# Performance work log

Measured on AMD Instinct MI355X. Metric: run time of the kernel, lower is better.

The kernel has to match this reference:

```python
import jax, jax.numpy as jnp
import numpy as np

N_NODES = 100000


def _gcn_norm(edge_index, num_nodes):
    # PyG gcn_norm with add_self_loops=True, symmetric normalization.
    src = jnp.concatenate([edge_index[0], jnp.arange(num_nodes)])
    dst = jnp.concatenate([edge_index[1], jnp.arange(num_nodes)])
    ones = jnp.ones(src.shape[0], dtype=jnp.float32)
    deg = jax.ops.segment_sum(ones, dst, num_segments=num_nodes)
    dinv = jnp.where(deg > 0, jax.lax.rsqrt(deg), 0.0)
    norm = dinv[src] * dinv[dst]  # [E + N]
    return src, dst, norm


def _gcn_conv(x, W, b, src, dst, norm, num_nodes):
    h = x @ W                                  # dense transform first (PyG order)
    msg = h[src] * norm[:, None]               # gather + scale, [E+N, D]
    agg = jax.ops.segment_sum(msg, dst, num_segments=num_nodes)
    return agg + b


def setup_inputs() -> dict:
    key = jax.random.key(0)
    ks = jax.random.split(key, 6)
    F_in, D, C, E = 256, 64, 47, 1200000
    x = jax.random.normal(ks[0], (N_NODES, F_in), dtype=jnp.float32)
    edge_index = jax.random.randint(ks[1], (2, E), 0, N_NODES)
    W1 = jax.random.normal(ks[2], (F_in, D), dtype=jnp.float32) * (1.0 / np.sqrt(F_in))
    b1 = jnp.zeros((D,), dtype=jnp.float32)
    W2 = jax.random.normal(ks[3], (D, C), dtype=jnp.float32) * (1.0 / np.sqrt(D))
    b2 = jnp.zeros((C,), dtype=jnp.float32)
    return {"x": x, "edge_index": edge_index, "W1": W1, "b1": b1, "W2": W2, "b2": b2}


def reference(x, edge_index, W1, b1, W2, b2):
    src, dst, norm = _gcn_norm(edge_index, N_NODES)
    h = jax.nn.relu(_gcn_conv(x, W1, b1, src, dst, norm, N_NODES))
    # dropout: eval mode (training=False) -> identity
    out = _gcn_conv(h, W2, b2, src, dst, norm, N_NODES)
    return jax.nn.log_softmax(out, axis=1)
```

## Files before the change

kernel.cpp:

```cpp
#include <hip/hip_runtime.h>
#include <math.h>

#define NN 100000
#define FIN 256
#define D1 64
#define C2 47
#define S2 48
#define NBKT 1563
#define CAP 1024
#define EPB 4096

typedef unsigned short u16;
typedef unsigned int u32;
typedef __attribute__((ext_vector_type(8))) short short8;
typedef __attribute__((ext_vector_type(4))) float floatx4;

__device__ __forceinline__ u16 f2b(float f) {
    union { float f; unsigned u; } v; v.f = f;
    unsigned r = v.u + 0x7FFF + ((v.u >> 16) & 1);
    return (u16)(r >> 16);
}
__device__ __forceinline__ float b2f_lo(u32 p) { union { unsigned u; float f; } v; v.u = p << 16; return v.f; }
__device__ __forceinline__ float b2f_hi(u32 p) { union { unsigned u; float f; } v; v.u = p & 0xFFFF0000u; return v.f; }
__device__ __forceinline__ u32 scale2(u32 pair, float dd) {
    return (u32)f2b(dd * b2f_lo(pair)) | ((u32)f2b(dd * b2f_hi(pair)) << 16);
}

__global__ __launch_bounds__(256) void k_pre(
    const float* __restrict__ W1, const float* __restrict__ W2,
    u16* __restrict__ W1t, u16* __restrict__ W2t, int* __restrict__ bucketCnt)
{
    int i = blockIdx.x * 256 + threadIdx.x;
    if (i < FIN * D1) {
        int c = i >> 8, k = i & 255;
        W1t[i] = f2b(W1[k * D1 + c]);
    } else if (i < FIN * D1 + D1 * S2) {
        int j = i - FIN * D1;
        int c = j >> 6, k = j & 63;
        W2t[j] = (c < C2) ? f2b(W2[k * C2 + c]) : (u16)0;
    } else {
        int z = i - (FIN * D1 + D1 * S2);
        if (z < NBKT) bucketCnt[z] = 0;
    }
}

__global__ __launch_bounds__(256) void k_bin_gemm1(
    const int* __restrict__ src, const int* __restrict__ dst, int E, int nScat,
    int* __restrict__ bucketCnt, u32* __restrict__ ebuf,
    const float* __restrict__ x, const u16* __restrict__ W1t,
    u16* __restrict__ h1u)
{
    __shared__ __align__(16) char smraw[20480];
    const int b = blockIdx.x;
    const int t = threadIdx.x;

    if (b < nScat) {
        int* hist = (int*)smraw;
        int* base = (int*)(smraw + 6256);
        for (int i = t; i < NBKT; i += 256) hist[i] = 0;
        __syncthreads();
        int e0 = b * EPB + t;
        u32 pk[16]; int bk[16], tk[16];
        #pragma unroll
        for (int j = 0; j < 16; ++j) {
            int e = e0 + j * 256;
            bk[j] = -1;
            if (e < E) {
                int d = dst[e];
                bk[j] = d >> 6;
                pk[j] = (u32)src[e] | ((u32)(d & 63) << 17);
                tk[j] = atomicAdd(&hist[bk[j]], 1);
            }
        }
        __syncthreads();
        for (int i = t; i < NBKT; i += 256)
            base[i] = hist[i] ? atomicAdd(&bucketCnt[i], hist[i]) : 0;
        __syncthreads();
        #pragma unroll
        for (int j = 0; j < 16; ++j)
            if (bk[j] >= 0) {
                int pos = base[bk[j]] + tk[j];
                if (pos < CAP) ebuf[(size_t)bk[j] * CAP + pos] = pk[j];
            }
        return;
    }

    short (*As)[2560] = (short(*)[2560])(smraw);
    short (*Bs)[2560] = (short(*)[2560])(smraw + 10240);
    const int bm = (b - nScat) * 64;
    const int w = t >> 6, lane = t & 63;
    const int arow = t >> 2;
    const int ak0 = (t & 3) * 8;

    floatx4 acc[4] = {};
    const int gr = bm + arow;
    const bool rowok = gr < NN;
    const float* xrow = x + (size_t)(rowok ? gr : 0) * FIN + ak0;

    float4 v0 = make_float4(0.f,0.f,0.f,0.f), v1 = v0;
    if (rowok) { v0 = *(const float4*)(xrow); v1 = *(const float4*)(xrow + 4); }
    short8 wv = *(const short8*)(W1t + arow * FIN + ak0);
    {
        short8 av;
        av[0]=(short)f2b(v0.x); av[1]=(short)f2b(v0.y); av[2]=(short)f2b(v0.z); av[3]=(short)f2b(v0.w);
        av[4]=(short)f2b(v1.x); av[5]=(short)f2b(v1.y); av[6]=(short)f2b(v1.z); av[7]=(short)f2b(v1.w);
        *(short8*)(&As[0][arow * 40 + ak0]) = av;
        *(short8*)(&Bs[0][arow * 40 + ak0]) = wv;
    }
    __syncthreads();

    int cb_ = 0;
    for (int kt = 32; kt <= FIN; kt += 32) {
        const bool more = kt < FIN;
        float4 n0, n1; short8 nw;
        if (more) {
            if (rowok) { n0 = *(const float4*)(xrow + kt); n1 = *(const float4*)(xrow + kt + 4); }
            else { n0 = make_float4(0.f,0.f,0.f,0.f); n1 = n0; }
            nw = *(const short8*)(W1t + arow * FIN + kt + ak0);
        }
        short8 af = *(const short8*)(&As[cb_][(w * 16 + (lane & 15)) * 40 + (lane >> 4) * 8]);
        #pragma unroll
        for (int cb = 0; cb < 4; ++cb) {
            short8 bv = *(const short8*)(&Bs[cb_][(cb * 16 + (lane & 15)) * 40 + (lane >> 4) * 8]);
            acc[cb] = __builtin_amdgcn_mfma_f32_16x16x32_bf16(af, bv, acc[cb], 0, 0, 0);
        }
        if (!more) break;
        short8 av;
        av[0]=(short)f2b(n0.x); av[1]=(short)f2b(n0.y); av[2]=(short)f2b(n0.z); av[3]=(short)f2b(n0.w);
        av[4]=(short)f2b(n1.x); av[5]=(short)f2b(n1.y); av[6]=(short)f2b(n1.z); av[7]=(short)f2b(n1.w);
        *(short8*)(&As[cb_ ^ 1][arow * 40 + ak0]) = av;
        *(short8*)(&Bs[cb_ ^ 1][arow * 40 + ak0]) = nw;
        __syncthreads();
        cb_ ^= 1;
    }

    #pragma unroll
    for (int cb = 0; cb < 4; ++cb) {
        #pragma unroll
        for (int r = 0; r < 4; ++r) {
            int grow = bm + w * 16 + (lane >> 4) * 4 + r;
            if (grow < NN)
                h1u[(size_t)grow * D1 + cb * 16 + (lane & 15)] = f2b(acc[cb][r]);
        }
    }
}

__global__ __launch_bounds__(256) void k_sort_scale(
    const int* __restrict__ bucketCnt, const u32* __restrict__ ebuf,
    int* __restrict__ rpg, u32* __restrict__ sortedg,
    const u16* __restrict__ h1u, u16* __restrict__ hs1)
{
    __shared__ int hist[64], cur[64];
    __shared__ float dinvs[64];
    const int b = blockIdx.x, t = threadIdx.x, bm = b * 64;

    if (t < 64) hist[t] = 0;
    __syncthreads();
    int cnt = bucketCnt[b]; if (cnt > CAP) cnt = CAP;
    const u32* eb = ebuf + (size_t)b * CAP;
    u32 p[4];
    #pragma unroll
    for (int j = 0; j < 4; ++j) {
        int e = t + j * 256;
        p[j] = 0xFFFFFFFFu;
        if (e < cnt) { p[j] = eb[e]; atomicAdd(&hist[(p[j] >> 17) & 63], 1); }
    }
    __syncthreads();
    if (t < 64) {
        int h = hist[t];
        int v = h;
        #pragma unroll
        for (int off = 1; off < 64; off <<= 1) {
            int u = __shfl_up(v, off);
            if (t >= off) v += u;
        }
        cur[t] = v - h;
        rpg[(size_t)b * 64 + t] = v - h;
        dinvs[t] = rsqrtf((float)h + 1.0f);
    }
    __syncthreads();
    #pragma unroll
    for (int j = 0; j < 4; ++j)
        if (p[j] != 0xFFFFFFFFu) {
            int pos = atomicAdd(&cur[(p[j] >> 17) & 63], 1);
            sortedg[(size_t)b * CAP + pos] = p[j] & 0x1FFFF;
        }

    const uint4* hb = (const uint4*)(h1u + (size_t)bm * D1);
    uint4* ob = (uint4*)(hs1 + (size_t)bm * D1);
    #pragma unroll
    for (int j = 0; j < 2; ++j) {
        int idx = t + j * 256;
        int row = idx >> 3;
        if (bm + row < NN) {
            uint4 v = hb[idx];
            float dd = dinvs[row];
            ob[idx] = make_uint4(scale2(v.x, dd), scale2(v.y, dd),
                                 scale2(v.z, dd), scale2(v.w, dd));
        }
    }
}

__global__ __launch_bounds__(256) void k_gather_gemm2(
    const int* __restrict__ bucketCnt, const int* __restrict__ rpg,
    const u32* __restrict__ sortedg, const u16* __restrict__ hs1,
    const float* __restrict__ b1, const u16* __restrict__ W2t,
    u16* __restrict__ hs2)
{
    __shared__ u32 sorted[CAP];
    __shared__ int rp[65];
    __shared__ short As[2][64 * 40];
    __shared__ short Bs[2][48 * 40];
    __shared__ float b1s[64];
    const int t = threadIdx.x;
    const int b = blockIdx.x, bm = b * 64;
    const int w = t >> 6, lane = t & 63;
    const int g = t >> 3, l8 = t & 7;

    for (int s = t; s < 384; s += 256) {
        int kt = s / 192, rem = s - kt * 192;
        int r = rem >> 2, j = rem & 3;
        *(short8*)(&Bs[kt][r * 40 + j * 8]) =
            *(const short8*)(W2t + r * D1 + kt * 32 + j * 8);
    }
    int cnt = bucketCnt[b]; if (cnt > CAP) cnt = CAP;
    if (t < 64) { b1s[t] = b1[t]; rp[t] = rpg[(size_t)b * 64 + t]; }
    if (t == 0) rp[64] = cnt;
    for (int i = t; i < cnt; i += 256)
        sorted[i] = sortedg[(size_t)b * CAP + i];
    __syncthreads();

    {
        const int col = 8 * l8;
        const int kth = l8 >> 2;
        const int cs  = col & 31;
        float4 bbl = *(const float4*)(b1s + col);
        float4 bbh = *(const float4*)(b1s + col + 4);
        #pragma unroll 1
        for (int i = 0; i < 2; ++i) {
            int rl = g * 2 + i;
            int node = bm + rl;
            if (node >= NN) break;
            int beg = rp[rl], end = rp[rl + 1];
            float dd = rsqrtf((float)(end - beg) + 1.0f);
            uint4 sp = *((const uint4*)(hs1 + (size_t)node * D1) + l8);
            float a0=b2f_lo(sp.x), a1=b2f_hi(sp.x), a2=b2f_lo(sp.y), a3=b2f_hi(sp.y);
            float a4=b2f_lo(sp.z), a5=b2f_hi(sp.z), a6=b2f_lo(sp.w), a7=b2f_hi(sp.w);
            float c0=0.f,c1=0.f,c2=0.f,c3=0.f,c4=0.f,c5=0.f,c6=0.f,c7=0.f;
            int e = beg;
            for (; e + 4 <= end; e += 4) {
                int s0 = sorted[e+0], s1 = sorted[e+1], s2 = sorted[e+2], s3 = sorted[e+3];
                uint4 p0 = *((const uint4*)(hs1 + (size_t)s0 * D1) + l8);
                uint4 p1 = *((const uint4*)(hs1 + (size_t)s1 * D1) + l8);
                uint4 p2 = *((const uint4*)(hs1 + (size_t)s2 * D1) + l8);
                uint4 p3 = *((const uint4*)(hs1 + (size_t)s3 * D1) + l8);
                a0+=b2f_lo(p0.x); a1+=b2f_hi(p0.x); a2+=b2f_lo(p0.y); a3+=b2f_hi(p0.y);
                a4+=b2f_lo(p0.z); a5+=b2f_hi(p0.z); a6+=b2f_lo(p0.w); a7+=b2f_hi(p0.w);
                c0+=b2f_lo(p1.x); c1+=b2f_hi(p1.x); c2+=b2f_lo(p1.y); c3+=b2f_hi(p1.y);
                c4+=b2f_lo(p1.z); c5+=b2f_hi(p1.z); c6+=b2f_lo(p1.w); c7+=b2f_hi(p1.w);
                a0+=b2f_lo(p2.x); a1+=b2f_hi(p2.x); a2+=b2f_lo(p2.y); a3+=b2f_hi(p2.y);
                a4+=b2f_lo(p2.z); a5+=b2f_hi(p2.z); a6+=b2f_lo(p2.w); a7+=b2f_hi(p2.w);
                c0+=b2f_lo(p3.x); c1+=b2f_hi(p3.x); c2+=b2f_lo(p3.y); c3+=b2f_hi(p3.y);
                c4+=b2f_lo(p3.z); c5+=b2f_hi(p3.z); c6+=b2f_lo(p3.w); c7+=b2f_hi(p3.w);
            }
            for (; e < end; ++e) {
                uint4 p0 = *((const uint4*)(hs1 + (size_t)sorted[e] * D1) + l8);
                a0+=b2f_lo(p0.x); a1+=b2f_hi(p0.x); a2+=b2f_lo(p0.y); a3+=b2f_hi(p0.y);
                a4+=b2f_lo(p0.z); a5+=b2f_hi(p0.z); a6+=b2f_lo(p0.w); a7+=b2f_hi(p0.w);
            }
            float r0 = fmaxf(fmaf(dd, a0 + c0, bbl.x), 0.f);
            float r1 = fmaxf(fmaf(dd, a1 + c1, bbl.y), 0.f);
            float r2 = fmaxf(fmaf(dd, a2 + c2, bbl.z), 0.f);
            float r3 = fmaxf(fmaf(dd, a3 + c3, bbl.w), 0.f);
            float r4 = fmaxf(fmaf(dd, a4 + c4, bbh.x), 0.f);
            float r5 = fmaxf(fmaf(dd, a5 + c5, bbh.y), 0.f);
            float r6 = fmaxf(fmaf(dd, a6 + c6, bbh.z), 0.f);
            float r7 = fmaxf(fmaf(dd, a7 + c7, bbh.w), 0.f);
            short8 pk;
            pk[0]=(short)f2b(r0); pk[1]=(short)f2b(r1); pk[2]=(short)f2b(r2); pk[3]=(short)f2b(r3);
            pk[4]=(short)f2b(r4); pk[5]=(short)f2b(r5); pk[6]=(short)f2b(r6); pk[7]=(short)f2b(r7);
            *(short8*)(&As[kth][rl * 40 + cs]) = pk;
        }
    }
    __syncthreads();

    floatx4 acc2[3] = {};
    #pragma unroll
    for (int kt = 0; kt < 2; ++kt) {
        short8 af = *(const short8*)(&As[kt][(w * 16 + (lane & 15)) * 40 + (lane >> 4) * 8]);
        #pragma unroll
        for (int cb = 0; cb < 3; ++cb) {
            short8 bv = *(const short8*)(&Bs[kt][(cb * 16 + (lane & 15)) * 40 + (lane >> 4) * 8]);
            acc2[cb] = __builtin_amdgcn_mfma_f32_16x16x32_bf16(af, bv, acc2[cb], 0, 0, 0);
        }
    }

    #pragma unroll
    for (int r = 0; r < 4; ++r) {
        int rl2 = w * 16 + (lane >> 4) * 4 + r;
        int grow = bm + rl2;
        if (grow < NN) {
            float dd2 = rsqrtf((float)(rp[rl2 + 1] - rp[rl2]) + 1.0f);
            #pragma unroll
            for (int cb = 0; cb < 3; ++cb) {
                float v = acc2[cb][r] * dd2;
                hs2[(size_t)grow * S2 + cb * 16 + (lane & 15)] = f2b(v);
            }
        }
    }
}

__global__ __launch_bounds__(256) void k_gather47(
    const int* __restrict__ bucketCnt, const int* __restrict__ rpg,
    const u32* __restrict__ sortedg, const u16* __restrict__ hs2,
    const float* __restrict__ b2, float* __restrict__ out)
{
    __shared__ u32 sorted[CAP];
    __shared__ int rp[65];
    __shared__ float b2s[48];
    const int t = threadIdx.x;
    const int b = blockIdx.x, bm = b * 64;
    const int g = t >> 3, l8 = t & 7;

    int cnt = bucketCnt[b]; if (cnt > CAP) cnt = CAP;
    if (t < 64) rp[t] = rpg[(size_t)b * 64 + t];
    if (t < 48) b2s[t] = (t < C2) ? b2[t] : 0.f;
    if (t == 0) rp[64] = cnt;
    for (int i = t; i < cnt; i += 256)
        sorted[i] = sortedg[(size_t)b * CAP + i];
    __syncthreads();

    const bool act = l8 < 6;
    const int lc = act ? l8 : 0;
    #pragma unroll 1
    for (int i = 0; i < 2; ++i) {
        int rl = g * 2 + i;
        int node = bm + rl;
        if (node >= NN) break;
        int beg = rp[rl], end = rp[rl + 1];
        float dd = rsqrtf((float)(end - beg) + 1.0f);
        uint4 sp = *((const uint4*)(hs2 + (size_t)node * S2) + lc);
        float a0=b2f_lo(sp.x), a1=b2f_hi(sp.x), a2=b2f_lo(sp.y), a3=b2f_hi(sp.y);
        float a4=b2f_lo(sp.z), a5=b2f_hi(sp.z), a6=b2f_lo(sp.w), a7=b2f_hi(sp.w);
        float c0=0.f,c1=0.f,c2=0.f,c3=0.f,c4=0.f,c5=0.f,c6=0.f,c7=0.f;
        int e = beg;
        for (; e + 4 <= end; e += 4) {
            int s0 = sorted[e+0], s1 = sorted[e+1], s2 = sorted[e+2], s3 = sorted[e+3];
            uint4 p0 = *((const uint4*)(hs2 + (size_t)s0 * S2) + lc);
            uint4 p1 = *((const uint4*)(hs2 + (size_t)s1 * S2) + lc);
            uint4 p2 = *((const uint4*)(hs2 + (size_t)s2 * S2) + lc);
            uint4 p3 = *((const uint4*)(hs2 + (size_t)s3 * S2) + lc);
            a0+=b2f_lo(p0.x); a1+=b2f_hi(p0.x); a2+=b2f_lo(p0.y); a3+=b2f_hi(p0.y);
            a4+=b2f_lo(p0.z); a5+=b2f_hi(p0.z); a6+=b2f_lo(p0.w); a7+=b2f_hi(p0.w);
            c0+=b2f_lo(p1.x); c1+=b2f_hi(p1.x); c2+=b2f_lo(p1.y); c3+=b2f_hi(p1.y);
            c4+=b2f_lo(p1.z); c5+=b2f_hi(p1.z); c6+=b2f_lo(p1.w); c7+=b2f_hi(p1.w);
            a0+=b2f_lo(p2.x); a1+=b2f_hi(p2.x); a2+=b2f_lo(p2.y); a3+=b2f_hi(p2.y);
            a4+=b2f_lo(p2.z); a5+=b2f_hi(p2.z); a6+=b2f_lo(p2.w); a7+=b2f_hi(p2.w);
            c0+=b2f_lo(p3.x); c1+=b2f_hi(p3.x); c2+=b2f_lo(p3.y); c3+=b2f_hi(p3.y);
            c4+=b2f_lo(p3.z); c5+=b2f_hi(p3.z); c6+=b2f_lo(p3.w); c7+=b2f_hi(p3.w);
        }
        for (; e < end; ++e) {
            uint4 p0 = *((const uint4*)(hs2 + (size_t)sorted[e] * S2) + lc);
            a0+=b2f_lo(p0.x); a1+=b2f_hi(p0.x); a2+=b2f_lo(p0.y); a3+=b2f_hi(p0.y);
            a4+=b2f_lo(p0.z); a5+=b2f_hi(p0.z); a6+=b2f_lo(p0.w); a7+=b2f_hi(p0.w);
        }
        float fv[8] = { a0+c0, a1+c1, a2+c2, a3+c3, a4+c4, a5+c5, a6+c6, a7+c7 };
        const int fb = 8 * lc;
        float val[8];
        float m = -INFINITY;
        #pragma unroll
        for (int k = 0; k < 8; ++k) {
            int fe = fb + k;
            bool valid = act && (fe < C2);
            val[k] = valid ? fmaf(dd, fv[k], b2s[valid ? fe : 0]) : -INFINITY;
            m = fmaxf(m, val[k]);
        }
        #pragma unroll
        for (int off = 1; off < 8; off <<= 1) m = fmaxf(m, __shfl_xor(m, off));
        float ex = 0.f;
        #pragma unroll
        for (int k = 0; k < 8; ++k)
            if (val[k] > -INFINITY) ex += expf(val[k] - m);
        #pragma unroll
        for (int off = 1; off < 8; off <<= 1) ex += __shfl_xor(ex, off);
        float ls = m + logf(ex);
        #pragma unroll
        for (int k = 0; k < 8; ++k) {
            int fe = fb + k;
            if (act && fe < C2) out[(size_t)node * C2 + fe] = val[k] - ls;
        }
    }
}

extern "C" void kernel_launch(void* const* d_in, const int* in_sizes, int n_in,
                              void* d_out, int out_size, void* d_ws, size_t ws_size,
                              hipStream_t stream) {
    const float* x  = (const float*)d_in[0];
    const int*   ei = (const int*)d_in[1];
    const float* W1 = (const float*)d_in[2];
    const float* b1 = (const float*)d_in[3];
    const float* W2 = (const float*)d_in[4];
    const float* b2 = (const float*)d_in[5];
    float* out = (float*)d_out;

    const int E = in_sizes[1] / 2;
    const int* src = ei;
    const int* dst = ei + E;

    char* ws = (char*)d_ws;
    int*   bucketCnt = (int*)(ws);
    u16*   W1t       = (u16*)(ws + 0x10000);
    u16*   W2t       = (u16*)(ws + 0x19000);
    int*   rpg       = (int*)(ws + 0x20000);
    u32*   ebuf      = (u32*)(ws + 0x100000);
    u32*   sortedg   = (u32*)(ws + 0x800000);
    u16*   h1u       = (u16*)(ws + 0xF00000);
    u16*   hs1       = (u16*)(ws + 0x1C00000);
    u16*   hs2       = (u16*)(ws + 0x2900000);

    const int nBk1 = (E + EPB - 1) / EPB;
    const int preB = (FIN * D1 + D1 * S2 + NBKT + 255) / 256;

    k_pre<<<preB, 256, 0, stream>>>(W1, W2, W1t, W2t, bucketCnt);
    k_bin_gemm1<<<nBk1 + NBKT, 256, 0, stream>>>(src, dst, E, nBk1,
                                                 bucketCnt, ebuf, x, W1t, h1u);
    k_sort_scale<<<NBKT, 256, 0, stream>>>(bucketCnt, ebuf, rpg, sortedg, h1u, hs1);
    k_gather_gemm2<<<NBKT, 256, 0, stream>>>(bucketCnt, rpg, sortedg, hs1, b1, W2t, hs2);
    k_gather47<<<NBKT, 256, 0, stream>>>(bucketCnt, rpg, sortedg, hs2, b2, out);
}
```

Baseline: 116.9 us.

## Load GEMM1 MFMA operands directly from global memory, dropping LDS staging

The GEMM1 path no longer stages x and W1t tiles through double-buffered shared memory with barriers. Each lane now loads its MFMA A fragment straight from x, converting to bf16 in registers, and reads B fragments from W1t in global memory (small and cache-resident), with the k-loop fully unrolled. This removes LDS writes, reads and __syncthreads. The cost is less coalesced global loads for x, since each lane reads 32 bytes per row at a 1 KB stride, and redundant W1t reads across waves. Shared memory shrinks to only the scatter histograms, which may raise occupancy for the fused kernel.

```diff
diff --git a/kernel.cpp b/kernel.cpp
--- a/kernel.cpp
+++ b/kernel.cpp
@@ -50,13 +50,12 @@
     const float* __restrict__ x, const u16* __restrict__ W1t,
     u16* __restrict__ h1u)
 {
-    __shared__ __align__(16) char smraw[20480];
+    __shared__ int hist[NBKT];
+    __shared__ int base[NBKT];
     const int b = blockIdx.x;
     const int t = threadIdx.x;
 
     if (b < nScat) {
-        int* hist = (int*)smraw;
-        int* base = (int*)(smraw + 6256);
         for (int i = t; i < NBKT; i += 256) hist[i] = 0;
         __syncthreads();
         int e0 = b * EPB + t;
@@ -85,53 +84,33 @@
         return;
     }
 
-    short (*As)[2560] = (short(*)[2560])(smraw);
-    short (*Bs)[2560] = (short(*)[2560])(smraw + 10240);
     const int bm = (b - nScat) * 64;
     const int w = t >> 6, lane = t & 63;
-    const int arow = t >> 2;
-    const int ak0 = (t & 3) * 8;
+    const int r16 = lane & 15;
+    const int kq = (lane >> 4) * 8;
+    const int row = bm + w * 16 + r16;
+    const bool rowok = row < NN;
+    const float* xrow = x + (size_t)(rowok ? row : 0) * FIN + kq;
+    const u16* wbase = W1t + (size_t)r16 * FIN + kq;
 
     floatx4 acc[4] = {};
-    const int gr = bm + arow;
-    const bool rowok = gr < NN;
-    const float* xrow = x + (size_t)(rowok ? gr : 0) * FIN + ak0;
-
-    float4 v0 = make_float4(0.f,0.f,0.f,0.f), v1 = v0;
-    if (rowok) { v0 = *(const float4*)(xrow); v1 = *(const float4*)(xrow + 4); }
-    short8 wv = *(const short8*)(W1t + arow * FIN + ak0);
-    {
-        short8 av;
-        av[0]=(short)f2b(v0.x); av[1]=(short)f2b(v0.y); av[2]=(short)f2b(v0.z); av[3]=(short)f2b(v0.w);
-        av[4]=(short)f2b(v1.x); av[5]=(short)f2b(v1.y); av[6]=(short)f2b(v1.z); av[7]=(short)f2b(v1.w);
-        *(short8*)(&As[0][arow * 40 + ak0]) = av;
-        *(short8*)(&Bs[0][arow * 40 + ak0]) = wv;
-    }
-    __syncthreads();
-
-    int cb_ = 0;
-    for (int kt = 32; kt <= FIN; kt += 32) {
-        const bool more = kt < FIN;
-        float4 n0, n1; short8 nw;
-        if (more) {
-            if (rowok) { n0 = *(const float4*)(xrow + kt); n1 = *(const float4*)(xrow + kt + 4); }
-            else { n0 = make_float4(0.f,0.f,0.f,0.f); n1 = n0; }
-            nw = *(const short8*)(W1t + arow * FIN + kt + ak0);
-        }
-        short8 af = *(const short8*)(&As[cb_][(w * 16 + (lane & 15)) * 40 + (lane >> 4) * 8]);
+    #pragma unroll
+    for (int kt = 0; kt < FIN; kt += 32) {
+        float4 v0 = make_float4(0.f,0.f,0.f,0.f), v1 = v0;
+        if (rowok) {
+            v0 = *(const float4*)(xrow + kt);
+            v1 = *(const float4*)(xrow + kt + 4);
+        }
+        short8 af;
+        af[0]=(short)f2b(v0.x); af[1]=(short)f2b(v0.y);
+        af[2]=(short)f2b(v0.z); af[3]=(short)f2b(v0.w);
+        af[4]=(short)f2b(v1.x); af[5]=(short)f2b(v1.y);
+        af[6]=(short)f2b(v1.z); af[7]=(short)f2b(v1.w);
         #pragma unroll
         for (int cb = 0; cb < 4; ++cb) {
-            short8 bv = *(const short8*)(&Bs[cb_][(cb * 16 + (lane & 15)) * 40 + (lane >> 4) * 8]);
+            short8 bv = *(const short8*)(wbase + (size_t)cb * 16 * FIN + kt);
             acc[cb] = __builtin_amdgcn_mfma_f32_16x16x32_bf16(af, bv, acc[cb], 0, 0, 0);
         }
-        if (!more) break;
-        short8 av;
-        av[0]=(short)f2b(n0.x); av[1]=(short)f2b(n0.y); av[2]=(short)f2b(n0.z); av[3]=(short)f2b(n0.w);
-        av[4]=(short)f2b(n1.x); av[5]=(short)f2b(n1.y); av[6]=(short)f2b(n1.z); av[7]=(short)f2b(n1.w);
-        *(short8*)(&As[cb_ ^ 1][arow * 40 + ak0]) = av;
-        *(short8*)(&Bs[cb_ ^ 1][arow * 40 + ak0]) = nw;
-        __syncthreads();
-        cb_ ^= 1;
     }
 
     #pragma unroll
@@ -140,7 +119,7 @@
         for (int r = 0; r < 4; ++r) {
             int grow = bm + w * 16 + (lane >> 4) * 4 + r;
             if (grow < NN)
-                h1u[(size_t)grow * D1 + cb * 16 + (lane & 15)] = f2b(acc[cb][r]);
+                h1u[(size_t)grow * D1 + cb * 16 + r16] = f2b(acc[cb][r]);
         }
     }
 }
```

Measured after the change: 135.4 us. +15.9%, slower.

## Triple-buffer GEMM1 shared tiles with two-deep register prefetch

Applied to the files above, without the earlier changes.

Rewrites the GEMM1 K-loop into a fully unrolled 3-stage LDS ring, with global loads issued two K-tiles ahead into alternating register sets. The aim is to hide global-memory latency for the x and W1 tile loads behind the MFMA work. It costs more shared memory per block (30KB instead of 20KB) and more registers, which may lower occupancy for both the scatter and GEMM blocks of this fused kernel.

```diff
diff --git a/kernel.cpp b/kernel.cpp
--- a/kernel.cpp
+++ b/kernel.cpp
@@ -50,7 +50,7 @@
     const float* __restrict__ x, const u16* __restrict__ W1t,
     u16* __restrict__ h1u)
 {
-    __shared__ __align__(16) char smraw[20480];
+    __shared__ __align__(16) char smraw[30720];
     const int b = blockIdx.x;
     const int t = threadIdx.x;
 
@@ -85,8 +85,8 @@
         return;
     }
 
-    short (*As)[2560] = (short(*)[2560])(smraw);
-    short (*Bs)[2560] = (short(*)[2560])(smraw + 10240);
+#define ASBUF(i) ((short*)(smraw + (i) * 5120))
+#define BSBUF(i) ((short*)(smraw + 15360 + (i) * 5120))
     const int bm = (b - nScat) * 64;
     const int w = t >> 6, lane = t & 63;
     const int arow = t >> 2;
@@ -97,41 +97,48 @@
     const bool rowok = gr < NN;
     const float* xrow = x + (size_t)(rowok ? gr : 0) * FIN + ak0;
 
-    float4 v0 = make_float4(0.f,0.f,0.f,0.f), v1 = v0;
-    if (rowok) { v0 = *(const float4*)(xrow); v1 = *(const float4*)(xrow + 4); }
-    short8 wv = *(const short8*)(W1t + arow * FIN + ak0);
-    {
+    auto LOADT = [&](int kt, float4& v0, float4& v1, short8& wv) {
+        if (rowok) { v0 = *(const float4*)(xrow + kt); v1 = *(const float4*)(xrow + kt + 4); }
+        else { v0 = make_float4(0.f,0.f,0.f,0.f); v1 = v0; }
+        wv = *(const short8*)(W1t + arow * FIN + kt + ak0);
+    };
+    auto WRITET = [&](short* As_, short* Bs_, const float4& v0, const float4& v1,
+                      const short8& wv) {
         short8 av;
         av[0]=(short)f2b(v0.x); av[1]=(short)f2b(v0.y); av[2]=(short)f2b(v0.z); av[3]=(short)f2b(v0.w);
         av[4]=(short)f2b(v1.x); av[5]=(short)f2b(v1.y); av[6]=(short)f2b(v1.z); av[7]=(short)f2b(v1.w);
-        *(short8*)(&As[0][arow * 40 + ak0]) = av;
-        *(short8*)(&Bs[0][arow * 40 + ak0]) = wv;
-    }
-    __syncthreads();
-
-    int cb_ = 0;
-    for (int kt = 32; kt <= FIN; kt += 32) {
-        const bool more = kt < FIN;
-        float4 n0, n1; short8 nw;
-        if (more) {
-            if (rowok) { n0 = *(const float4*)(xrow + kt); n1 = *(const float4*)(xrow + kt + 4); }
-            else { n0 = make_float4(0.f,0.f,0.f,0.f); n1 = n0; }
-            nw = *(const short8*)(W1t + arow * FIN + kt + ak0);
-        }
-        short8 af = *(const short8*)(&As[cb_][(w * 16 + (lane & 15)) * 40 + (lane >> 4) * 8]);
+        *(short8*)(&As_[arow * 40 + ak0]) = av;
+        *(short8*)(&Bs_[arow * 40 + ak0]) = wv;
+    };
+    auto MFMAT = [&](const short* As_, const short* Bs_) {
+        short8 af = *(const short8*)(&As_[(w * 16 + (lane & 15)) * 40 + (lane >> 4) * 8]);
         #pragma unroll
         for (int cb = 0; cb < 4; ++cb) {
-            short8 bv = *(const short8*)(&Bs[cb_][(cb * 16 + (lane & 15)) * 40 + (lane >> 4) * 8]);
+            short8 bv = *(const short8*)(&Bs_[(cb * 16 + (lane & 15)) * 40 + (lane >> 4) * 8]);
             acc[cb] = __builtin_amdgcn_mfma_f32_16x16x32_bf16(af, bv, acc[cb], 0, 0, 0);
         }
-        if (!more) break;
-        short8 av;
-        av[0]=(short)f2b(n0.x); av[1]=(short)f2b(n0.y); av[2]=(short)f2b(n0.z); av[3]=(short)f2b(n0.w);
-        av[4]=(short)f2b(n1.x); av[5]=(short)f2b(n1.y); av[6]=(short)f2b(n1.z); av[7]=(short)f2b(n1.w);
-        *(short8*)(&As[cb_ ^ 1][arow * 40 + ak0]) = av;
-        *(short8*)(&Bs[cb_ ^ 1][arow * 40 + ak0]) = nw;
-        __syncthreads();
-        cb_ ^= 1;
+    };
+
+    float4 s0v0, s0v1; short8 s0w;
+    float4 s1v0, s1v1; short8 s1w;
+
+    LOADT(0,  s1v0, s1v1, s1w);
+    LOADT(32, s0v0, s0v1, s0w);
+    WRITET(ASBUF(0), BSBUF(0), s1v0, s1v1, s1w);
+    __syncthreads();
+
+    #pragma unroll
+    for (int i = 0; i < 8; ++i) {
+        if (i + 2 < 8) {
+            if ((i + 1) & 1) LOADT((i + 2) * 32, s1v0, s1v1, s1w);
+            else             LOADT((i + 2) * 32, s0v0, s0v1, s0w);
+        }
+        MFMAT(ASBUF(i % 3), BSBUF(i % 3));
+        if (i + 1 < 8) {
+            if (i & 1) WRITET(ASBUF((i + 1) % 3), BSBUF((i + 1) % 3), s1v0, s1v1, s1w);
+            else       WRITET(ASBUF((i + 1) % 3), BSBUF((i + 1) % 3), s0v0, s0v1, s0w);
+            __syncthreads();
+        }
     }
 
     #pragma unroll
@@ -143,6 +150,8 @@
                 h1u[(size_t)grow * D1 + cb * 16 + (lane & 15)] = f2b(acc[cb][r]);
         }
     }
+#undef ASBUF
+#undef BSBUF
 }
 
 __global__ __launch_bounds__(256) void k_sort_scale(
```

Measured after the change: 116.9 us. About the same (+0.0%).
